# Performance work log

Hardware: AMD Instinct MI355X
Metric: run time of the kernel (lower is better)

## Reference

```python
import jax, jax.numpy as jnp
import numpy as np

N = 100000
E = 1600000
IN_DIM = 128
HID = 128
OUT_DIM = 128


def _glorot(key, shape):
    lim = jnp.sqrt(6.0 / (shape[0] + shape[1]))
    return jax.random.uniform(key, shape, jnp.float32, -lim, lim)


def setup_inputs() -> dict:
    key = jax.random.key(0)
    ks = jax.random.split(key, 8)
    x = jax.random.normal(ks[0], (N, IN_DIM), jnp.float32)
    edge_index = jax.random.randint(ks[1], (2, E), 0, N, jnp.int64)
    # layer 1 (SAGEConv(in_dim, hid)): lin_l applied to mean-aggregated neighbors (with bias),
    # lin_r applied to root features (no bias) -- PyG SAGEConv semantics.
    W1l = _glorot(ks[2], (IN_DIM, HID))
    b1l = jnp.zeros((HID,), jnp.float32)
    W1r = _glorot(ks[3], (IN_DIM, HID))
    # layer 2 (SAGEConv(hid, out_dim))
    W2l = _glorot(ks[4], (HID, OUT_DIM))
    b2l = jnp.zeros((OUT_DIM,), jnp.float32)
    W2r = _glorot(ks[5], (HID, OUT_DIM))
    return {"x": x, "edge_index": edge_index,
            "W1l": W1l, "b1l": b1l, "W1r": W1r,
            "W2l": W2l, "b2l": b2l, "W2r": W2r}


def _sage_conv(h, src, dst, Wl, bl, Wr):
    # mean aggregation of source features onto target nodes
    msg_sum = jax.ops.segment_sum(h[src], dst, num_segments=N)  # [N, d]
    deg = jax.ops.segment_sum(jnp.ones((src.shape[0],), h.dtype), dst, num_segments=N)
    agg = msg_sum / jnp.maximum(deg, 1.0)[:, None]
    return agg @ Wl + bl + h @ Wr


def reference(x, edge_index, W1l, b1l, W1r, W2l, b2l, W2r):
    src = edge_index[0]
    dst = edge_index[1]
    h = jax.nn.relu(_sage_conv(x, src, dst, W1l, b1l, W1r))
    h = _sage_conv(h, src, dst, W2l, b2l, W2r)
    return h
```

## Files before the change

kernel.cpp:

```cpp
#include <hip/hip_runtime.h>
#include <cstdint>
#include <cstddef>

#define NN 100000
#define EE 1600000
#define DIM 128
#define CAP 48
#define OVF_CAP 512

#define NB 391
#define BCAP 4608
#define SLOTS 32
#define FLUSH_AT 16
#define ACHUNK 4096
#define ATHREADS 512

#define NPREP_W 128
#define NPREP_X ((NN * DIM / 4) / ATHREADS)

#if __has_builtin(__builtin_amdgcn_cvt_pk_f32_fp8) && __has_builtin(__builtin_amdgcn_cvt_pk_fp8_f32)
#define HAVE_FP8 1
#else
#define HAVE_FP8 0
#endif

typedef __attribute__((ext_vector_type(8))) short bf16x8;
typedef __attribute__((ext_vector_type(4))) float f32x4;
typedef __attribute__((ext_vector_type(2))) float f32x2;

__device__ __forceinline__ unsigned short f2bf(float f) {
  union { float f; uint32_t u; } v; v.f = f;
  uint32_t r = v.u + 0x7FFF + ((v.u >> 16) & 1);
  return (unsigned short)(r >> 16);
}
__device__ __forceinline__ uint32_t pk2(float a, float b) {
  return (uint32_t)f2bf(a) | ((uint32_t)f2bf(b) << 16);
}

template <bool HI>
__device__ __forceinline__ uint32_t f2fp8_pair(float a, float b, uint32_t old) {
#if HAVE_FP8
  return (uint32_t)__builtin_amdgcn_cvt_pk_fp8_f32(a, b, (int)old, HI);
#else
  auto enc = [](float f) -> uint32_t {
    union { float f; uint32_t u; } v; v.f = f;
    uint32_t s = (v.u >> 31) << 7;
    uint32_t m = v.u & 0x7FFFFFFF;
    if (m < 0x3C000000u) {
      union { uint32_t u; float f; } w; w.u = m;
      int q = (int)(w.f * 512.0f + 0.5f);
      if (q > 7) return s | (1u << 3);
      return s | (uint32_t)q;
    }
    uint32_t u2 = m + 0x00080000u;
    int e = (int)(u2 >> 23) - 127;
    if (e > 8) return s | 0x7E;
    return s | ((uint32_t)(e + 7) << 3) | ((u2 >> 20) & 7);
  };
  uint32_t pr = enc(a) | (enc(b) << 8);
  return HI ? ((old & 0x0000FFFFu) | (pr << 16)) : ((old & 0xFFFF0000u) | pr);
#endif
}

__device__ __forceinline__ void acc_fp8x8(float* s, uint2 w) {
#if HAVE_FP8
  f32x2 f;
  f = __builtin_amdgcn_cvt_pk_f32_fp8((int)w.x, false); s[0] += f.x; s[1] += f.y;
  f = __builtin_amdgcn_cvt_pk_f32_fp8((int)w.x, true);  s[2] += f.x; s[3] += f.y;
  f = __builtin_amdgcn_cvt_pk_f32_fp8((int)w.y, false); s[4] += f.x; s[5] += f.y;
  f = __builtin_amdgcn_cvt_pk_f32_fp8((int)w.y, true);  s[6] += f.x; s[7] += f.y;
#else
  auto dec = [](uint32_t b) -> float {
    uint32_t sg = (b >> 7) & 1, e = (b >> 3) & 15, m = b & 7;
    if (e == 0) return (sg ? -1.f : 1.f) * (float)m * 0.001953125f;
    union { uint32_t u; float f; } w;
    w.u = (sg << 31) | ((e + 120) << 23) | (m << 20);
    return w.f;
  };
#pragma unroll
  for (int i = 0; i < 4; ++i) s[i] += dec((w.x >> (i * 8)) & 0xFF);
#pragma unroll
  for (int i = 0; i < 4; ++i) s[4 + i] += dec((w.y >> (i * 8)) & 0xFF);
#endif
}

__global__ __launch_bounds__(ATHREADS) void partA_prep_kernel(
    const void* __restrict__ edges, int* __restrict__ bcnt,
    unsigned* __restrict__ part, int* __restrict__ novf, int* __restrict__ ovf,
    const float* __restrict__ x,
    const float* __restrict__ W1l, const float* __restrict__ W1r,
    const float* __restrict__ W2l, const float* __restrict__ W2r,
    unsigned short* __restrict__ Wt1, unsigned short* __restrict__ Wt2,
    unsigned short* __restrict__ xb, unsigned char* __restrict__ x8) {
  __shared__ unsigned stage[NB][SLOTS + 1];
  __shared__ int scnt[NB];
  __shared__ int sh_i64;
  const int t = threadIdx.x;

  if (blockIdx.x >= NB) {
    int bid = blockIdx.x - NB;
    if (bid < NPREP_W) {
      int idx = bid * ATHREADS + t;
      int layer = idx >> 15;
      int rest = idx & 32767;
      int mat = rest >> 14;
      int r = rest & 16383;
      int k = r >> 7, n = r & 127;
      const float* W = layer ? (mat ? W2r : W2l) : (mat ? W1r : W1l);
      unsigned short* Wt = layer ? Wt2 : Wt1;
      Wt[((size_t)(mat * 128 + n)) * 128 + k] = f2bf(W[k * 128 + n]);
    } else {
      int i = (bid - NPREP_W) * ATHREADS + t;
      if (i < NN * DIM / 4) {
        f32x4 v = ((const f32x4*)x)[i];
        ushort4 hb;
        hb.x = f2bf(v[0]); hb.y = f2bf(v[1]); hb.z = f2bf(v[2]); hb.w = f2bf(v[3]);
        ((ushort4*)xb)[i] = hb;
        uint32_t pk = f2fp8_pair<false>(v[0], v[1], 0);
        pk = f2fp8_pair<true>(v[2], v[3], pk);
        ((uint32_t*)x8)[i] = pk;
      }
    }
    return;
  }

  for (int b = t; b < NB; b += ATHREADS) scnt[b] = 0;
  if (t < 64) {
    int v = ((const int*)edges)[2 * t + 1];
    unsigned long long m = __ballot(v != 0);
    if (t == 0) sh_i64 = (m == 0ull) ? 1 : 0;
  }
  __syncthreads();
  const int i64 = sh_i64;
  const long long ebase = (long long)blockIdx.x * ACHUNK;
  const int nrounds = ACHUNK / ATHREADS;
  for (int r = 0; r < nrounds; ++r) {
    long long e = ebase + (long long)r * ATHREADS + t;
    if (e < EE) {
      int s, d;
      if (i64) {
        s = (int)((const long long*)edges)[e];
        d = (int)((const long long*)edges)[(long long)EE + e];
      } else {
        s = ((const int*)edges)[e];
        d = ((const int*)edges)[(long long)EE + e];
      }
      if ((unsigned)s < NN && (unsigned)d < NN) {
        int b = d >> 8;
        unsigned pk = (unsigned)s | ((unsigned)(d & 255) << 17);
        int pos = atomicAdd(&scnt[b], 1);
        if (pos < SLOTS) {
          stage[b][pos] = pk;
        } else {
          int g = atomicAdd(&bcnt[b], 1);
          if (g < BCAP) part[(size_t)b * BCAP + g] = pk;
          else { int oi = atomicAdd(novf, 1); if (oi < OVF_CAP) { ovf[oi*2] = s; ovf[oi*2+1] = d; } }
        }
      }
    }
    __syncthreads();
    const bool last = (r == nrounds - 1);
    for (int b = t; b < NB; b += ATHREADS) {
      int c = scnt[b];
      if (c > SLOTS) c = SLOTS;
      if (c > 0 && (last || c >= FLUSH_AT)) {
        int g = atomicAdd(&bcnt[b], c);
        for (int i = 0; i < c; ++i) {
          int gp = g + i;
          unsigned pk = stage[b][i];
          if (gp < BCAP) {
            part[(size_t)b * BCAP + gp] = pk;
          } else {
            int oi = atomicAdd(novf, 1);
            if (oi < OVF_CAP) { ovf[oi*2] = (int)(pk & 0x1FFFF); ovf[oi*2+1] = (b << 8) | (int)(pk >> 17); }
          }
        }
        scnt[b] = 0;
      }
    }
    __syncthreads();
  }
}

__global__ __launch_bounds__(256) void partB_kernel(
    const int* __restrict__ bcnt, const unsigned* __restrict__ part,
    int* __restrict__ cnt, int* __restrict__ ell,
    int* __restrict__ novf, int* __restrict__ ovf) {
  __shared__ int lcnt[256];
  __shared__ int lell[256 * CAP];
  const int t = threadIdx.x;
  const int b = blockIdx.x;
  lcnt[t] = 0;
  __syncthreads();
  int n = bcnt[b];
  if (n > BCAP) n = BCAP;
  for (int i = t; i < n; i += 256) {
    unsigned pk = part[(size_t)b * BCAP + i];
    int s = (int)(pk & 0x1FFFF);
    int dl = (int)(pk >> 17);
    int pos = atomicAdd(&lcnt[dl], 1);
    if (pos < CAP) lell[dl * CAP + pos] = s;
    else { int oi = atomicAdd(novf, 1); if (oi < OVF_CAP) { ovf[oi*2] = s; ovf[oi*2+1] = (b << 8) | dl; } }
  }
  __syncthreads();
  int4* dst = (int4*)(ell + (size_t)b * 256 * CAP);
  const int4* src = (const int4*)lell;
#pragma unroll
  for (int i = 0; i < 256 * CAP / 4 / 256; ++i) dst[t + i * 256] = src[t + i * 256];
  int node = b * 256 + t;
  if (node < NN) cnt[node] = lcnt[t];
}

__global__ __launch_bounds__(256) void gather_ell_kernel(
    const int* __restrict__ cnt, const int* __restrict__ ell,
    const unsigned char* __restrict__ h8, unsigned short* __restrict__ ahi,
    const int* __restrict__ novf, const int* __restrict__ ovf) {
  const int node = blockIdx.x * 4 + (threadIdx.x >> 6);
  const int lane = threadIdx.x & 63;
  const int q = lane >> 4;
  const int l = lane & 15;
  if (node >= NN) return;
  const int dcnt = cnt[node];
  const int n = dcnt < CAP ? dcnt : CAP;
  const int* row = ell + (size_t)node * CAP;
  float s[8] = {0.f, 0.f, 0.f, 0.f, 0.f, 0.f, 0.f, 0.f};
  int p = q;
  for (; p + 12 < n; p += 16) {
    uint2 w0 = *(const uint2*)(h8 + (size_t)row[p] * DIM + l * 8);
    uint2 w1 = *(const uint2*)(h8 + (size_t)row[p + 4] * DIM + l * 8);
    uint2 w2 = *(const uint2*)(h8 + (size_t)row[p + 8] * DIM + l * 8);
    uint2 w3 = *(const uint2*)(h8 + (size_t)row[p + 12] * DIM + l * 8);
    acc_fp8x8(s, w0);
    acc_fp8x8(s, w1);
    acc_fp8x8(s, w2);
    acc_fp8x8(s, w3);
  }
  for (; p < n; p += 4) {
    uint2 w0 = *(const uint2*)(h8 + (size_t)row[p] * DIM + l * 8);
    acc_fp8x8(s, w0);
  }
#pragma unroll
  for (int i = 0; i < 8; ++i) {
    s[i] += __shfl_xor(s[i], 16, 64);
    s[i] += __shfl_xor(s[i], 32, 64);
  }
  if (q == 0) {
    if (dcnt > CAP) {
      int no = *novf;
      if (no > OVF_CAP) no = OVF_CAP;
      for (int i = 0; i < no; ++i) {
        if (ovf[i * 2 + 1] == node) {
          uint2 w0 = *(const uint2*)(h8 + (size_t)ovf[i * 2] * DIM + l * 8);
          acc_fp8x8(s, w0);
        }
      }
    }
    const float rd = 1.0f / fmaxf((float)dcnt, 1.0f);
    uint4 o;
    o.x = pk2(s[0] * rd, s[1] * rd);
    o.y = pk2(s[2] * rd, s[3] * rd);
    o.z = pk2(s[4] * rd, s[5] * rd);
    o.w = pk2(s[6] * rd, s[7] * rd);
    *(uint4*)(ahi + (size_t)node * DIM + l * 8) = o;
  }
}

template <bool RELU, bool WP, bool WOUT>
__global__ __launch_bounds__(256, 2) void dense_mfma_kernel(
    const unsigned short* __restrict__ ahi, unsigned short* hb,
    const unsigned short* __restrict__ Wt, const float* __restrict__ bl,
    float* __restrict__ out, unsigned char* ph8, int n) {
  const int t = threadIdx.x;
  const int wave = t >> 6, lane = t & 63;
  const int l15 = lane & 15, l4 = lane >> 4;
  const int base = blockIdx.x * 64;

  bf16x8 bfr[2][4][2];
#pragma unroll
  for (int mat = 0; mat < 2; ++mat)
#pragma unroll
    for (int kt = 0; kt < 4; ++kt)
#pragma unroll
      for (int ntl = 0; ntl < 2; ++ntl) {
        int ncol = (wave * 2 + ntl) * 16 + l15;
        int k0 = kt * 32 + l4 * 8;
        bfr[mat][kt][ntl] = *(const bf16x8*)(Wt + ((size_t)(mat * 128 + ncol)) * 128 + k0);
      }

  f32x4 acc[4][2];
#pragma unroll
  for (int ntl = 0; ntl < 2; ++ntl) {
    float b = bl[(wave * 2 + ntl) * 16 + l15];
#pragma unroll
    for (int rt = 0; rt < 4; ++rt) {
      f32x4 ib = {b, b, b, b};
      acc[rt][ntl] = ib;
    }
  }

#pragma unroll
  for (int kt = 0; kt < 4; ++kt) {
    const int k0 = kt * 32 + l4 * 8;
#pragma unroll
    for (int rt = 0; rt < 4; ++rt) {
      int row = base + rt * 16 + l15;
      if (row >= n) row = n - 1;
      const size_t off = (size_t)row * DIM + k0;
      bf16x8 a8 = *(const bf16x8*)(ahi + off);
      bf16x8 hh8 = *(const bf16x8*)(hb + off);
#pragma unroll
      for (int ntl = 0; ntl < 2; ++ntl) {
        acc[rt][ntl] = __builtin_amdgcn_mfma_f32_16x16x32_bf16(a8, bfr[0][kt][ntl], acc[rt][ntl], 0, 0, 0);
        acc[rt][ntl] = __builtin_amdgcn_mfma_f32_16x16x32_bf16(hh8, bfr[1][kt][ntl], acc[rt][ntl], 0, 0, 0);
      }
    }
  }

  __syncthreads();

#pragma unroll
  for (int rt = 0; rt < 4; ++rt)
#pragma unroll
    for (int ntl = 0; ntl < 2; ++ntl) {
      const int col = (wave * 2 + ntl) * 16 + l15;
#pragma unroll
      for (int r = 0; r < 4; ++r) {
        int row = base + rt * 16 + l4 * 4 + r;
        if (row < n) {
          float v = acc[rt][ntl][r];
          if (RELU) v = fmaxf(v, 0.f);
          const size_t off = (size_t)row * DIM + col;
          if (WOUT) out[off] = v;
          if (WP) {
            hb[off] = f2bf(v);
            ph8[off] = (unsigned char)(f2fp8_pair<false>(v, v, 0) & 0xFF);
          }
        }
      }
    }
}

extern "C" void kernel_launch(void* const* d_in, const int* in_sizes, int n_in,
                              void* d_out, int out_size, void* d_ws, size_t ws_size,
                              hipStream_t stream) {
  const float* x   = (const float*)d_in[0];
  const void* edges = d_in[1];
  const float* W1l = (const float*)d_in[2];
  const float* b1l = (const float*)d_in[3];
  const float* W1r = (const float*)d_in[4];
  const float* W2l = (const float*)d_in[5];
  const float* b2l = (const float*)d_in[6];
  const float* W2r = (const float*)d_in[7];
  float* out = (float*)d_out;

  char* p = (char*)d_ws;
  unsigned short* Wt1 = (unsigned short*)p;               p += 2 * 128 * 128 * 2;
  unsigned short* Wt2 = (unsigned short*)p;               p += 2 * 128 * 128 * 2;
  int* cnt  = (int*)p;                                    p += (size_t)NN * 4;
  int* bcnt = (int*)p;                                    p += (size_t)NB * 4;
  int* novf = (int*)p;                                    p += 4;
  p = (char*)(((uintptr_t)p + 15) & ~(uintptr_t)15);
  int* ovf = (int*)p;                                     p += (size_t)OVF_CAP * 2 * 4;
  p = (char*)(((uintptr_t)p + 255) & ~(uintptr_t)255);
  int* ell = (int*)p;                                     p += (size_t)NB * 256 * CAP * 4;
  p = (char*)(((uintptr_t)p + 255) & ~(uintptr_t)255);
  unsigned short* ahi = (unsigned short*)p;               p += (size_t)NN * DIM * 2;
  unsigned short* hb = (unsigned short*)p;                p += (size_t)NN * DIM * 2;
  unsigned char* h8 = (unsigned char*)p;                  p += (size_t)NN * DIM;
  unsigned* part = (unsigned*)ahi;

  (void)hipMemsetAsync(bcnt, 0, ((size_t)NB + 1) * 4, stream);

  partA_prep_kernel<<<NB + NPREP_W + NPREP_X, ATHREADS, 0, stream>>>(
      edges, bcnt, part, novf, ovf, x, W1l, W1r, W2l, W2r, Wt1, Wt2, hb, h8);
  partB_kernel<<<NB, 256, 0, stream>>>(bcnt, part, cnt, ell, novf, ovf);

  const int gather_blocks = (NN + 3) / 4;
  const int dense_blocks = (NN + 63) / 64;

  gather_ell_kernel<<<gather_blocks, 256, 0, stream>>>(cnt, ell, h8, ahi, novf, ovf);
  dense_mfma_kernel<true, true, false><<<dense_blocks, 256, 0, stream>>>(
      ahi, hb, Wt1, b1l, out, h8, NN);

  gather_ell_kernel<<<gather_blocks, 256, 0, stream>>>(cnt, ell, h8, ahi, novf, ovf);
  dense_mfma_kernel<false, false, true><<<dense_blocks, 256, 0, stream>>>(
      ahi, hb, Wt2, b2l, out, nullptr, NN);
}
```

Baseline: 230.7 us.

## Replace global-atomic edge bucketing with per-block fixed-size bucket segments

The edge partition pass stops staging edges in LDS and reserving space with global atomics per bucket. Instead, each edge block writes straight into its own fixed segment of SEG entries per destination bucket and records a per-(bucket, block) count. The second pass walks those segments to build the ELL lists. This removes the global atomics, the repeated flush rounds with barriers, and the bcnt memset. In exchange, partB reads are less coalesced, with a serial per-thread walk over segments. Any block that sends more than SEG edges to one bucket spills into the small overflow list.

```diff
diff --git a/kernel.cpp b/kernel.cpp
--- a/kernel.cpp
+++ b/kernel.cpp
@@ -9,10 +9,9 @@
 #define OVF_CAP 512
 
 #define NB 391
-#define BCAP 4608
-#define SLOTS 32
-#define FLUSH_AT 16
 #define ACHUNK 4096
+#define EDGE_BLKS 391
+#define SEG 40
 #define ATHREADS 512
 
 #define NPREP_W 128
@@ -85,20 +84,19 @@
 }
 
 __global__ __launch_bounds__(ATHREADS) void partA_prep_kernel(
-    const void* __restrict__ edges, int* __restrict__ bcnt,
+    const void* __restrict__ edges, int* __restrict__ bcnt2,
     unsigned* __restrict__ part, int* __restrict__ novf, int* __restrict__ ovf,
     const float* __restrict__ x,
     const float* __restrict__ W1l, const float* __restrict__ W1r,
     const float* __restrict__ W2l, const float* __restrict__ W2r,
     unsigned short* __restrict__ Wt1, unsigned short* __restrict__ Wt2,
     unsigned short* __restrict__ xb, unsigned char* __restrict__ x8) {
-  __shared__ unsigned stage[NB][SLOTS + 1];
-  __shared__ int scnt[NB];
+  __shared__ int cnt391[NB];
   __shared__ int sh_i64;
   const int t = threadIdx.x;
 
-  if (blockIdx.x >= NB) {
-    int bid = blockIdx.x - NB;
+  if (blockIdx.x >= EDGE_BLKS) {
+    int bid = blockIdx.x - EDGE_BLKS;
     if (bid < NPREP_W) {
       int idx = bid * ATHREADS + t;
       int layer = idx >> 15;
@@ -124,7 +122,7 @@
     return;
   }
 
-  for (int b = t; b < NB; b += ATHREADS) scnt[b] = 0;
+  for (int b = t; b < NB; b += ATHREADS) cnt391[b] = 0;
   if (t < 64) {
     int v = ((const int*)edges)[2 * t + 1];
     unsigned long long m = __ballot(v != 0);
@@ -133,8 +131,8 @@
   __syncthreads();
   const int i64 = sh_i64;
   const long long ebase = (long long)blockIdx.x * ACHUNK;
-  const int nrounds = ACHUNK / ATHREADS;
-  for (int r = 0; r < nrounds; ++r) {
+#pragma unroll
+  for (int r = 0; r < ACHUNK / ATHREADS; ++r) {
     long long e = ebase + (long long)r * ATHREADS + t;
     if (e < EE) {
       int s, d;
@@ -148,42 +146,25 @@
       if ((unsigned)s < NN && (unsigned)d < NN) {
         int b = d >> 8;
         unsigned pk = (unsigned)s | ((unsigned)(d & 255) << 17);
-        int pos = atomicAdd(&scnt[b], 1);
-        if (pos < SLOTS) {
-          stage[b][pos] = pk;
+        int pos = atomicAdd(&cnt391[b], 1);
+        if (pos < SEG) {
+          part[((size_t)b * EDGE_BLKS + blockIdx.x) * SEG + pos] = pk;
         } else {
-          int g = atomicAdd(&bcnt[b], 1);
-          if (g < BCAP) part[(size_t)b * BCAP + g] = pk;
-          else { int oi = atomicAdd(novf, 1); if (oi < OVF_CAP) { ovf[oi*2] = s; ovf[oi*2+1] = d; } }
+          int oi = atomicAdd(novf, 1);
+          if (oi < OVF_CAP) { ovf[oi * 2] = s; ovf[oi * 2 + 1] = d; }
         }
       }
     }
-    __syncthreads();
-    const bool last = (r == nrounds - 1);
-    for (int b = t; b < NB; b += ATHREADS) {
-      int c = scnt[b];
-      if (c > SLOTS) c = SLOTS;
-      if (c > 0 && (last || c >= FLUSH_AT)) {
-        int g = atomicAdd(&bcnt[b], c);
-        for (int i = 0; i < c; ++i) {
-          int gp = g + i;
-          unsigned pk = stage[b][i];
-          if (gp < BCAP) {
-            part[(size_t)b * BCAP + gp] = pk;
-          } else {
-            int oi = atomicAdd(novf, 1);
-            if (oi < OVF_CAP) { ovf[oi*2] = (int)(pk & 0x1FFFF); ovf[oi*2+1] = (b << 8) | (int)(pk >> 17); }
-          }
-        }
-        scnt[b] = 0;
-      }
-    }
-    __syncthreads();
+  }
+  __syncthreads();
+  for (int b = t; b < NB; b += ATHREADS) {
+    int c = cnt391[b];
+    bcnt2[(size_t)b * EDGE_BLKS + blockIdx.x] = c < SEG ? c : SEG;
   }
 }
 
 __global__ __launch_bounds__(256) void partB_kernel(
-    const int* __restrict__ bcnt, const unsigned* __restrict__ part,
+    const int* __restrict__ bcnt2, const unsigned* __restrict__ part,
     int* __restrict__ cnt, int* __restrict__ ell,
     int* __restrict__ novf, int* __restrict__ ovf) {
   __shared__ int lcnt[256];
@@ -192,15 +173,17 @@
   const int b = blockIdx.x;
   lcnt[t] = 0;
   __syncthreads();
-  int n = bcnt[b];
-  if (n > BCAP) n = BCAP;
-  for (int i = t; i < n; i += 256) {
-    unsigned pk = part[(size_t)b * BCAP + i];
-    int s = (int)(pk & 0x1FFFF);
-    int dl = (int)(pk >> 17);
-    int pos = atomicAdd(&lcnt[dl], 1);
-    if (pos < CAP) lell[dl * CAP + pos] = s;
-    else { int oi = atomicAdd(novf, 1); if (oi < OVF_CAP) { ovf[oi*2] = s; ovf[oi*2+1] = (b << 8) | dl; } }
+  for (int blk = t; blk < EDGE_BLKS; blk += 256) {
+    int c = bcnt2[(size_t)b * EDGE_BLKS + blk];
+    const unsigned* seg = part + ((size_t)b * EDGE_BLKS + blk) * SEG;
+    for (int i = 0; i < c; ++i) {
+      unsigned pk = seg[i];
+      int s = (int)(pk & 0x1FFFF);
+      int dl = (int)(pk >> 17);
+      int pos = atomicAdd(&lcnt[dl], 1);
+      if (pos < CAP) lell[dl * CAP + pos] = s;
+      else { int oi = atomicAdd(novf, 1); if (oi < OVF_CAP) { ovf[oi*2] = s; ovf[oi*2+1] = (b << 8) | dl; } }
+    }
   }
   __syncthreads();
   int4* dst = (int4*)(ell + (size_t)b * 256 * CAP);
@@ -356,9 +339,9 @@
   char* p = (char*)d_ws;
   unsigned short* Wt1 = (unsigned short*)p;               p += 2 * 128 * 128 * 2;
   unsigned short* Wt2 = (unsigned short*)p;               p += 2 * 128 * 128 * 2;
-  int* cnt  = (int*)p;                                    p += (size_t)NN * 4;
-  int* bcnt = (int*)p;                                    p += (size_t)NB * 4;
-  int* novf = (int*)p;                                    p += 4;
+  int* cnt   = (int*)p;                                   p += (size_t)NN * 4;
+  int* bcnt2 = (int*)p;                                   p += (size_t)NB * EDGE_BLKS * 4;
+  int* novf  = (int*)p;                                   p += 4;
   p = (char*)(((uintptr_t)p + 15) & ~(uintptr_t)15);
   int* ovf = (int*)p;                                     p += (size_t)OVF_CAP * 2 * 4;
   p = (char*)(((uintptr_t)p + 255) & ~(uintptr_t)255);
@@ -369,11 +352,11 @@
   unsigned char* h8 = (unsigned char*)p;                  p += (size_t)NN * DIM;
   unsigned* part = (unsigned*)ahi;
 
-  (void)hipMemsetAsync(bcnt, 0, ((size_t)NB + 1) * 4, stream);
-
-  partA_prep_kernel<<<NB + NPREP_W + NPREP_X, ATHREADS, 0, stream>>>(
-      edges, bcnt, part, novf, ovf, x, W1l, W1r, W2l, W2r, Wt1, Wt2, hb, h8);
-  partB_kernel<<<NB, 256, 0, stream>>>(bcnt, part, cnt, ell, novf, ovf);
+  (void)hipMemsetAsync(novf, 0, 4, stream);
+
+  partA_prep_kernel<<<EDGE_BLKS + NPREP_W + NPREP_X, ATHREADS, 0, stream>>>(
+      edges, bcnt2, part, novf, ovf, x, W1l, W1r, W2l, W2r, Wt1, Wt2, hb, h8);
+  partB_kernel<<<NB, 256, 0, stream>>>(bcnt2, part, cnt, ell, novf, ovf);
 
   const int gather_blocks = (NN + 3) / 4;
   const int dense_blocks = (NN + 63) / 64;
```

Result: slower. 235.5 us (+2.1%).
